# Kernel tuning notes

Measured on AMD Instinct MI355X. Metric: run time of the kernel, lower is better.

## Reference

```python
import jax, jax.numpy as jnp
import numpy as np

B, D = 4096, 128
LU, LI = 10, 20
NU, NI = 100000, 100000
NFU, NFI = 2000, 5000
MARGIN = 1.0


def setup_inputs() -> dict:
    key = jax.random.key(0)
    ks = jax.random.split(key, 32)
    s = 0.05
    n = lambda i, shape: (jax.random.normal(ks[i], shape, dtype=jnp.float32) * s)
    inp = {
        'user_indices': jax.random.randint(ks[0], (B,), 0, NU),
        'user_feat': jax.random.randint(ks[1], (B, LU), 0, NFU),
        'pos_item_indices': jax.random.randint(ks[2], (B,), 0, NI),
        'pos_item_feat': jax.random.randint(ks[3], (B, LI), 0, NFI),
        'neg_item_indices': jax.random.randint(ks[4], (B, 1), 0, NI),
        'neg_item_feat': jax.random.randint(ks[5], (B, 1, LI), 0, NFI),
        'comp_neg_indices': jax.random.randint(ks[6], (B,), 0, NI),
        'eps': jax.random.normal(ks[7], (B, D), dtype=jnp.float32),
        # learned parameters
        'emb_user': n(8, (NU, D)),
        'emb_item': n(9, (NI, D)),
        'emb_feat_user': n(10, (NFU, D)).at[0].set(0.0),  # row 0 is padding
        'emb_feat_item': n(11, (NFI, D)).at[0].set(0.0),
        'pop_emb_user': n(12, (D,)),
        'int_emb_user': n(13, (D,)),
        'pop_emb_item': n(14, (D,)),
        'int_emb_item': n(15, (D,)),
        'W_pop': n(16, (D, D)), 'b_pop': jnp.zeros((D,), jnp.float32),
        'W_int': n(17, (D, D)), 'b_int': jnp.zeros((D,), jnp.float32),
        'enc_W': n(18, (LI * D, D)), 'enc_b': jnp.zeros((D,), jnp.float32),
        'dec_W': n(19, (D, LI * D)), 'dec_b': jnp.zeros((LI * D,), jnp.float32),
        'fc11_W': n(20, (D, D)), 'fc11_b': jnp.zeros((D,), jnp.float32),
        'fc12_W': n(21, (D, D)), 'fc12_b': jnp.zeros((D,), jnp.float32),
    }
    return inp


def _attend_pool(fuse, feat_mask, vec, W, b):
    # fuse: [B, L+1, D], feat_mask: [B, L+1] (int, 0 = padded)
    scores = jnp.einsum('bld,d->bl', fuse, vec)
    scores = jnp.where(feat_mask == 0, -jnp.inf, scores)
    w = jax.nn.softmax(scores, axis=1)
    pooled = jnp.einsum('bld,bl->bd', fuse, w)
    return pooled @ W + b


def _branch(idx, feat, emb_table, feat_table, pop_vec, int_vec, W_pop, b_pop, W_int, b_int):
    e = emb_table[idx]                       # [B, D]
    fe = feat_table[feat]                    # [B, L, D]
    fuse = jnp.concatenate([e[:, None, :], fe], axis=1)           # [B, L+1, D]
    ones = jnp.ones((idx.shape[0], 1), dtype=feat.dtype)
    mask = jnp.concatenate([ones, feat], axis=1)                  # [B, L+1]
    hot = _attend_pool(fuse, mask, pop_vec, W_pop, b_pop)
    cold = _attend_pool(fuse, mask, int_vec, W_int, b_int)
    return hot, cold, e, fe


def reference(user_indices, user_feat, pos_item_indices, pos_item_feat,
              neg_item_indices, neg_item_feat, comp_neg_indices, eps,
              emb_user, emb_item, emb_feat_user, emb_feat_item,
              pop_emb_user, int_emb_user, pop_emb_item, int_emb_item,
              W_pop, b_pop, W_int, b_int,
              enc_W, enc_b, dec_W, dec_b, fc11_W, fc11_b, fc12_W, fc12_b):
    neg_item_indices = neg_item_indices.squeeze(1)
    neg_item_feat = neg_item_feat.squeeze(1)

    u_hot, u_cold, _, _ = _branch(user_indices, user_feat, emb_user, emb_feat_user,
                                  pop_emb_user, int_emb_user, W_pop, b_pop, W_int, b_int)
    p_hot, p_cold, pos_e, pos_fe = _branch(pos_item_indices, pos_item_feat, emb_item, emb_feat_item,
                                           pop_emb_item, int_emb_item, W_pop, b_pop, W_int, b_int)
    n_hot, n_cold, _, _ = _branch(neg_item_indices, neg_item_feat, emb_item, emb_feat_item,
                                  pop_emb_item, int_emb_item, W_pop, b_pop, W_int, b_int)

    loss_hot = jax.nn.relu(jnp.sum((u_hot - p_hot) ** 2, -1)
                           - jnp.sum((u_hot - n_hot) ** 2, -1) + MARGIN)
    loss_cold = jax.nn.relu(jnp.sum((u_cold - p_cold) ** 2, -1)
                            - jnp.sum((u_cold - n_cold) ** 2, -1) + MARGIN)

    # VAE over positive item feature embeddings
    x = pos_fe.reshape(pos_fe.shape[0], LI * D)
    h1 = jax.nn.relu(x @ enc_W + enc_b)
    mu = h1 @ fc11_W + fc11_b
    logvar = h1 @ fc12_W + fc12_b
    z = eps * jnp.exp(0.5 * logvar) + mu
    recon = z @ dec_W + dec_b                                    # [B, LI*D]
    mse = jnp.sum((recon - x) ** 2)
    kld = -0.5 * jnp.sum(1.0 + logvar - mu ** 2 - jnp.exp(logvar))
    vae_l = mse / LI + kld

    comp_e = emb_item[comp_neg_indices]
    mmi = -jnp.sum(jax.nn.log_sigmoid(jnp.sum(z * pos_e, 1) - jnp.sum(z * comp_e, 1)))
    item_vae_loss = mmi + vae_l + jnp.sum((z - pos_e) ** 2)

    return loss_hot, loss_cold, item_vae_loss
```

## Files before the change

### kernel.cpp

```cpp
#include <hip/hip_runtime.h>
#include <math.h>

#define BATCH 4096
#define DIM 128
#define LU 10
#define LI 20

typedef float  f32x4  __attribute__((ext_vector_type(4)));
typedef short  s16x8  __attribute__((ext_vector_type(8)));

__device__ __forceinline__ short f2bf(float x) {
    unsigned u = __float_as_uint(x);
    u += 0x7FFFu + ((u >> 16) & 1u);
    return (short)(u >> 16);
}
__device__ __forceinline__ float bf2f(unsigned short u) {
    return __uint_as_float(((unsigned)u) << 16);
}

__global__ __launch_bounds__(256) void k_prep(
    const float* __restrict__ enc_W, const float* __restrict__ dec_W,
    const float* __restrict__ fc11_W, const float* __restrict__ fc12_W,
    const float* __restrict__ W_pop, const float* __restrict__ W_int,
    const float* __restrict__ ef_item, const float* __restrict__ ef_user,
    short* __restrict__ encWT, short* __restrict__ decWT,
    short* __restrict__ fc11WT, short* __restrict__ fc12WT,
    short* __restrict__ wpopT, short* __restrict__ wintT,
    short* __restrict__ ef16, short* __restrict__ efU16)
{
    __shared__ float tile[32][33];
    const int b = blockIdx.x;
    const int t = threadIdx.x;

    if (b < 704) {
        const float* src; short* dst; int r0, c0, src_ld, dst_ld;
        if (b < 320) {
            int tk = b % 80, tj = b / 80;
            src = enc_W; dst = encWT; r0 = tk * 32; c0 = tj * 32; src_ld = 128; dst_ld = 2560;
        } else if (b < 640) {
            int tb = b - 320; int tc = tb % 80, td = tb / 80;
            src = dec_W; dst = decWT; r0 = td * 32; c0 = tc * 32; src_ld = 2560; dst_ld = 128;
        } else if (b < 656) {
            int tb = b - 640; int tk = tb % 4, tj = tb / 4;
            src = fc11_W; dst = fc11WT; r0 = tk * 32; c0 = tj * 32; src_ld = 128; dst_ld = 128;
        } else if (b < 672) {
            int tb = b - 656; int tk = tb % 4, tj = tb / 4;
            src = fc12_W; dst = fc12WT; r0 = tk * 32; c0 = tj * 32; src_ld = 128; dst_ld = 128;
        } else if (b < 688) {
            int tb = b - 672; int tk = tb % 4, tj = tb / 4;
            src = W_pop; dst = wpopT; r0 = tk * 32; c0 = tj * 32; src_ld = 128; dst_ld = 128;
        } else {
            int tb = b - 688; int tk = tb % 4, tj = tb / 4;
            src = W_int; dst = wintT; r0 = tk * 32; c0 = tj * 32; src_ld = 128; dst_ld = 128;
        }
        for (int q = 0; q < 4; ++q) {
            int e = t + q * 256;
            int r = e >> 5, c = e & 31;
            tile[r][c] = src[(size_t)(r0 + r) * src_ld + (c0 + c)];
        }
        __syncthreads();
        for (int q = 0; q < 4; ++q) {
            int e = t + q * 256;
            int r = e >> 5, c = e & 31;
            dst[(size_t)(c0 + r) * dst_ld + (r0 + c)] = f2bf(tile[c][r]);
        }
    } else if (b < 1329) {
        int base = (b - 704) * 1024 + t * 4;
        float4 v = *(const float4*)(ef_item + base);
        short4 o;
        o.x = f2bf(v.x); o.y = f2bf(v.y); o.z = f2bf(v.z); o.w = f2bf(v.w);
        *(short4*)(ef16 + base) = o;
    } else {
        int base = (b - 1329) * 1024 + t * 4;
        float4 v = *(const float4*)(ef_user + base);
        short4 o;
        o.x = f2bf(v.x); o.y = f2bf(v.y); o.z = f2bf(v.z); o.w = f2bf(v.w);
        *(short4*)(efU16 + base) = o;
    }
}

template<int L>
__device__ __forceinline__ void pool_online(
    const int* __restrict__ idxp, const int* __restrict__ featp,
    const float* __restrict__ etab, const unsigned short* __restrict__ ftab16,
    const float* __restrict__ vpop, const float* __restrict__ vint,
    float* __restrict__ poolH, float* __restrict__ poolC,
    int i, int j32)
{
    const int d = j32 * 4;
    const float4 vp = *(const float4*)(vpop + d);
    const float4 vi = *(const float4*)(vint + d);

    int fidx[L];
#pragma unroll
    for (int l = 0; l < L; ++l) fidx[l] = featp[(size_t)i * L + l];

    const int idx = idxp[i];
    const float4 e0 = *(const float4*)(etab + (size_t)idx * DIM + d);

    float sH = e0.x * vp.x + e0.y * vp.y + e0.z * vp.z + e0.w * vp.w;
    float sC = e0.x * vi.x + e0.y * vi.y + e0.z * vi.z + e0.w * vi.w;
    sH += __shfl_xor(sH, 1, 64);  sC += __shfl_xor(sC, 1, 64);
    sH += __shfl_xor(sH, 2, 64);  sC += __shfl_xor(sC, 2, 64);
    sH += __shfl_xor(sH, 4, 64);  sC += __shfl_xor(sC, 4, 64);
    sH += __shfl_xor(sH, 8, 64);  sC += __shfl_xor(sC, 8, 64);
    sH += __shfl_xor(sH, 16, 64); sC += __shfl_xor(sC, 16, 64);

    float mH = sH, mC = sC;
    float sumH = 1.f, sumC = 1.f;
    float aHx = e0.x, aHy = e0.y, aHz = e0.z, aHw = e0.w;
    float aCx = e0.x, aCy = e0.y, aCz = e0.z, aCw = e0.w;

#pragma unroll
    for (int l = 0; l < L; ++l) {
        const int f = fidx[l];
        const ushort4 u = *(const ushort4*)(ftab16 + (size_t)f * DIM + d);
        const float rx = bf2f(u.x), ry = bf2f(u.y), rz = bf2f(u.z), rw = bf2f(u.w);

        float pH = rx * vp.x + ry * vp.y + rz * vp.z + rw * vp.w;
        float pC = rx * vi.x + ry * vi.y + rz * vi.z + rw * vi.w;
        pH += __shfl_xor(pH, 1, 64);  pC += __shfl_xor(pC, 1, 64);
        pH += __shfl_xor(pH, 2, 64);  pC += __shfl_xor(pC, 2, 64);
        pH += __shfl_xor(pH, 4, 64);  pC += __shfl_xor(pC, 4, 64);
        pH += __shfl_xor(pH, 8, 64);  pC += __shfl_xor(pC, 8, 64);
        pH += __shfl_xor(pH, 16, 64); pC += __shfl_xor(pC, 16, 64);

        const bool v = (f != 0);
        const float mH2 = v ? fmaxf(mH, pH) : mH;
        const float mC2 = v ? fmaxf(mC, pC) : mC;
        const float sclH = __expf(mH - mH2);
        const float sclC = __expf(mC - mC2);
        const float wH = v ? __expf(pH - mH2) : 0.f;
        const float wC = v ? __expf(pC - mC2) : 0.f;
        sumH = sumH * sclH + wH;
        sumC = sumC * sclC + wC;
        aHx = aHx * sclH + wH * rx;  aHy = aHy * sclH + wH * ry;
        aHz = aHz * sclH + wH * rz;  aHw = aHw * sclH + wH * rw;
        aCx = aCx * sclC + wC * rx;  aCy = aCy * sclC + wC * ry;
        aCz = aCz * sclC + wC * rz;  aCw = aCw * sclC + wC * rw;
        mH = mH2; mC = mC2;
    }

    const float rH = 1.f / sumH, rC = 1.f / sumC;
    float4 oH; oH.x = aHx * rH; oH.y = aHy * rH; oH.z = aHz * rH; oH.w = aHw * rH;
    float4 oC; oC.x = aCx * rC; oC.y = aCy * rC; oC.z = aCz * rC; oC.w = aCw * rC;
    *(float4*)(poolH + (size_t)i * DIM + d) = oH;
    *(float4*)(poolC + (size_t)i * DIM + d) = oC;
}

__global__ __launch_bounds__(256) void k_AB(
    const int* __restrict__ user_idx, const int* __restrict__ user_feat,
    const int* __restrict__ pos_idx,  const int* __restrict__ pos_feat,
    const int* __restrict__ neg_idx,  const int* __restrict__ neg_feat,
    const int* __restrict__ comp_idx,
    const float* __restrict__ emb_user, const float* __restrict__ emb_item,
    const float* __restrict__ pop_u, const float* __restrict__ int_u,
    const float* __restrict__ pop_i, const float* __restrict__ int_i,
    const float* __restrict__ eps,
    const float* __restrict__ enc_b,
    const float* __restrict__ fc11_b, const float* __restrict__ fc12_b,
    const short* __restrict__ encWT,
    const short* __restrict__ fc11WT, const short* __restrict__ fc12WT,
    const short* __restrict__ ef16, const short* __restrict__ efU16,
    float* __restrict__ pooled,
    short* __restrict__ zbuf, float* __restrict__ vae_part)
{
    __shared__ int   featsL[320];
    __shared__ int   spi[16], sci[16];
    __shared__ __align__(16) short hlds[2048];
    __shared__ float sdots[4][16][3];
    __shared__ float red[256];

    const int t    = threadIdx.x;
    const int w    = t >> 6;
    const int lane = t & 63;
    const int g    = lane >> 4;
    const int q    = lane & 15;
    const size_t SEC = (size_t)BATCH * DIM;

    if (blockIdx.x < 1536) {
        const int pb  = blockIdx.x;
        const int br  = pb >> 9;
        const int i   = (pb & 511) * 8 + (t >> 5);
        const int j32 = t & 31;
        if (br == 0) {
            pool_online<LU>(user_idx, user_feat, emb_user,
                            (const unsigned short*)efU16, pop_u, int_u,
                            pooled + 0 * SEC, pooled + 1 * SEC, i, j32);
        } else if (br == 1) {
            pool_online<LI>(pos_idx, pos_feat, emb_item,
                            (const unsigned short*)ef16, pop_i, int_i,
                            pooled + 2 * SEC, pooled + 3 * SEC, i, j32);
        } else {
            pool_online<LI>(neg_idx, neg_feat, emb_item,
                            (const unsigned short*)ef16, pop_i, int_i,
                            pooled + 4 * SEC, pooled + 5 * SEC, i, j32);
        }
        return;
    }

    const int sg = blockIdx.x - 1536;
    const int i0 = sg * 16;

    if (t < 16)      spi[t] = pos_idx[i0 + t];
    else if (t < 32) sci[t - 16] = comp_idx[i0 + t - 16];
    if (t < 256) featsL[t] = pos_feat[i0 * LI + t];
    if (t < 64)  featsL[256 + t] = pos_feat[i0 * LI + 256 + t];
    __syncthreads();

    const int j0 = w * 32 + q;
    const int j1 = j0 + 16;
    const short* bbase0 = encWT + (size_t)j0 * 2560 + g * 8;
    const short* bbase1 = encWT + (size_t)j1 * 2560 + g * 8;

    f32x4 acc0 = {0.f, 0.f, 0.f, 0.f};
    f32x4 acc1 = {0.f, 0.f, 0.f, 0.f};
    for (int l = 0; l < LI; ++l) {
        const int f = featsL[q * LI + l];
        const short* arow = ef16 + (size_t)f * DIM + g * 8;
#pragma unroll
        for (int dt = 0; dt < 4; ++dt) {
            const int koff = l * 128 + dt * 32;
            s16x8 a  = *(const s16x8*)(arow + dt * 32);
            s16x8 b0 = *(const s16x8*)(bbase0 + koff);
            s16x8 b1 = *(const s16x8*)(bbase1 + koff);
            acc0 = __builtin_amdgcn_mfma_f32_16x16x32_bf16(a, b0, acc0, 0, 0, 0);
            acc1 = __builtin_amdgcn_mfma_f32_16x16x32_bf16(a, b1, acc1, 0, 0, 0);
        }
    }

    {
        float eb0 = enc_b[j0], eb1 = enc_b[j1];
#pragma unroll
        for (int r = 0; r < 4; ++r) {
            int s = g * 4 + r;
            float h0 = acc0[r] + eb0; h0 = h0 > 0.f ? h0 : 0.f;
            float h1 = acc1[r] + eb1; h1 = h1 > 0.f ? h1 : 0.f;
            int swz = (s & 7) << 3;
            hlds[(s * 128 + j0) ^ swz] = f2bf(h0);
            hlds[(s * 128 + j1) ^ swz] = f2bf(h1);
        }
    }
    __syncthreads();

    const short* fb0_11 = fc11WT + (size_t)j0 * DIM + g * 8;
    const short* fb1_11 = fc11WT + (size_t)j1 * DIM + g * 8;
    const short* fb0_12 = fc12WT + (size_t)j0 * DIM + g * 8;
    const short* fb1_12 = fc12WT + (size_t)j1 * DIM + g * 8;

    f32x4 mu0 = {0.f,0.f,0.f,0.f}, mu1 = {0.f,0.f,0.f,0.f};
    f32x4 lv0 = {0.f,0.f,0.f,0.f}, lv1 = {0.f,0.f,0.f,0.f};
#pragma unroll
    for (int kt = 0; kt < 4; ++kt) {
        int sidx = (q * 128 + kt * 32 + g * 8) ^ ((q & 7) << 3);
        s16x8 a = *(const s16x8*)&hlds[sidx];
        s16x8 w11a = *(const s16x8*)(fb0_11 + kt * 32);
        s16x8 w11b = *(const s16x8*)(fb1_11 + kt * 32);
        s16x8 w12a = *(const s16x8*)(fb0_12 + kt * 32);
        s16x8 w12b = *(const s16x8*)(fb1_12 + kt * 32);
        mu0 = __builtin_amdgcn_mfma_f32_16x16x32_bf16(a, w11a, mu0, 0, 0, 0);
        mu1 = __builtin_amdgcn_mfma_f32_16x16x32_bf16(a, w11b, mu1, 0, 0, 0);
        lv0 = __builtin_amdgcn_mfma_f32_16x16x32_bf16(a, w12a, lv0, 0, 0, 0);
        lv1 = __builtin_amdgcn_mfma_f32_16x16x32_bf16(a, w12b, lv1, 0, 0, 0);
    }

    float b11_0 = fc11_b[j0], b11_1 = fc11_b[j1];
    float b12_0 = fc12_b[j0], b12_1 = fc12_b[j1];

    float kacc = 0.f;
#pragma unroll
    for (int r = 0; r < 4; ++r) {
        const int s = g * 4 + r;
        const int i = i0 + s;
        float m0 = mu0[r] + b11_0, m1 = mu1[r] + b11_1;
        float v0 = lv0[r] + b12_0, v1 = lv1[r] + b12_1;
        float e0 = eps[(size_t)i * DIM + j0];
        float e1 = eps[(size_t)i * DIM + j1];
        float z0 = e0 * expf(0.5f * v0) + m0;
        float z1 = e1 * expf(0.5f * v1) + m1;
        zbuf[(size_t)i * DIM + j0] = f2bf(z0);
        zbuf[(size_t)i * DIM + j1] = f2bf(z1);
        kacc += (1.f + v0 - m0 * m0 - expf(v0)) + (1.f + v1 - m1 * m1 - expf(v1));

        const size_t pb2 = (size_t)spi[s] * DIM;
        const size_t cb2 = (size_t)sci[s] * DIM;
        float pe0 = emb_item[pb2 + j0], pe1 = emb_item[pb2 + j1];
        float ce0 = emb_item[cb2 + j0], ce1 = emb_item[cb2 + j1];
        float zp = z0 * pe0 + z1 * pe1;
        float zc = z0 * ce0 + z1 * ce1;
        float d0 = z0 - pe0, d1 = z1 - pe1;
        float zq = d0 * d0 + d1 * d1;
        for (int mm = 8; mm >= 1; mm >>= 1) {
            zp += __shfl_xor(zp, mm, 64);
            zc += __shfl_xor(zc, mm, 64);
            zq += __shfl_xor(zq, mm, 64);
        }
        if (q == 0) {
            sdots[w][s][0] = zp;
            sdots[w][s][1] = zc;
            sdots[w][s][2] = zq;
        }
    }

    red[t] = -0.5f * kacc;
    __syncthreads();
    if (t < 16) {
        float zp = 0.f, zc = 0.f, zq = 0.f;
        for (int ww = 0; ww < 4; ++ww) {
            zp += sdots[ww][t][0];
            zc += sdots[ww][t][1];
            zq += sdots[ww][t][2];
        }
        float x = zp - zc;
        float ls = (x >= 0.f) ? -log1pf(expf(-x)) : (x - log1pf(expf(x)));
        red[t] += -ls + zq;
    }
    __syncthreads();
    for (int off = 128; off > 0; off >>= 1) {
        if (t < off) red[t] += red[t + off];
        __syncthreads();
    }
    if (t == 0) vae_part[sg] = red[0];
}

__global__ __launch_bounds__(256) void k_C(
    const float* __restrict__ pooled,
    const short* __restrict__ wpopT, const short* __restrict__ wintT,
    const int* __restrict__ pos_feat,
    const float* __restrict__ ef_item, const float* __restrict__ dec_b,
    const short* __restrict__ decWT, const short* __restrict__ zbuf,
    float* __restrict__ out_hot, float* __restrict__ out_cold,
    float* __restrict__ dec_part)
{
    __shared__ int   featsL[320];
    __shared__ float red[256];
    __shared__ float sArr[4][16];

    const int t    = threadIdx.x;
    const int w    = t >> 6;
    const int lane = t & 63;
    const int g    = lane >> 4;
    const int q    = lane & 15;

    if (blockIdx.x >= 2048) {
        const int i0 = (blockIdx.x - 2048) * 16;
        const int h     = w >> 1;
        const int other = (w & 1) + 1;
        const float* pu = pooled + (size_t)(0 * 2 + h) * BATCH * DIM;
        const float* po = pooled + (size_t)(other * 2 + h) * BATCH * DIM;
        const short* wT = h ? wintT : wpopT;

        s16x8 afr[4];
#pragma unroll
        for (int kt = 0; kt < 4; ++kt) {
            const size_t off = (size_t)(i0 + q) * DIM + kt * 32 + g * 8;
            f32x4 ua = *(const f32x4*)(pu + off);
            f32x4 ub = *(const f32x4*)(pu + off + 4);
            f32x4 oa = *(const f32x4*)(po + off);
            f32x4 ob = *(const f32x4*)(po + off + 4);
            s16x8 v;
            v[0] = f2bf(ua[0] - oa[0]); v[1] = f2bf(ua[1] - oa[1]);
            v[2] = f2bf(ua[2] - oa[2]); v[3] = f2bf(ua[3] - oa[3]);
            v[4] = f2bf(ub[0] - ob[0]); v[5] = f2bf(ub[1] - ob[1]);
            v[6] = f2bf(ub[2] - ob[2]); v[7] = f2bf(ub[3] - ob[3]);
            afr[kt] = v;
        }

        float sq0 = 0.f, sq1 = 0.f, sq2 = 0.f, sq3 = 0.f;
        for (int fr = 0; fr < 8; ++fr) {
            const short* bb = wT + (size_t)(fr * 16 + q) * DIM + g * 8;
            f32x4 acc = {0.f, 0.f, 0.f, 0.f};
#pragma unroll
            for (int kt = 0; kt < 4; ++kt) {
                s16x8 bfr = *(const s16x8*)(bb + kt * 32);
                acc = __builtin_amdgcn_mfma_f32_16x16x32_bf16(afr[kt], bfr, acc, 0, 0, 0);
            }
            sq0 += acc[0] * acc[0]; sq1 += acc[1] * acc[1];
            sq2 += acc[2] * acc[2]; sq3 += acc[3] * acc[3];
        }
        for (int m = 8; m >= 1; m >>= 1) {
            sq0 += __shfl_xor(sq0, m, 64);
            sq1 += __shfl_xor(sq1, m, 64);
            sq2 += __shfl_xor(sq2, m, 64);
            sq3 += __shfl_xor(sq3, m, 64);
        }
        if (q == 0) {
            sArr[w][g * 4 + 0] = sq0;
            sArr[w][g * 4 + 1] = sq1;
            sArr[w][g * 4 + 2] = sq2;
            sArr[w][g * 4 + 3] = sq3;
        }
        __syncthreads();
        if (t < 16) {
            float v = sArr[0][t] - sArr[1][t] + 1.0f;
            out_hot[i0 + t] = v > 0.f ? v : 0.f;
        } else if (t < 32) {
            int s = t - 16;
            float v = sArr[2][s] - sArr[3][s] + 1.0f;
            out_cold[i0 + s] = v > 0.f ? v : 0.f;
        }
        return;
    }

    const int db     = blockIdx.x;
    const int cchunk = db >> 8;
    const int sb     = db & 255;
    const int i0     = sb * 16;

    if (t < 256) featsL[t] = pos_feat[i0 * LI + t];
    if (t < 64)  featsL[256 + t] = pos_feat[i0 * LI + 256 + t];
    __syncthreads();

    s16x8 za[4];
#pragma unroll
    for (int kt = 0; kt < 4; ++kt)
        za[kt] = *(const s16x8*)(zbuf + (size_t)(i0 + q) * DIM + kt * 32 + g * 8);

    const int cw = cchunk * 320 + w * 80;

    s16x8 bb[5][4];
    float xs[5][4];
    float bias[5];
#pragma unroll
    for (int fp = 0; fp < 5; ++fp) {
        const int c = cw + fp * 16 + q;
        const short* bp = decWT + (size_t)c * DIM + g * 8;
#pragma unroll
        for (int kt = 0; kt < 4; ++kt)
            bb[fp][kt] = *(const s16x8*)(bp + kt * 32);
        const int l = c >> 7, dcol = c & 127;
#pragma unroll
        for (int r = 0; r < 4; ++r)
            xs[fp][r] = ef_item[(size_t)featsL[(g * 4 + r) * LI + l] * DIM + dcol];
        bias[fp] = dec_b[c];
    }

    float macc = 0.f;
#pragma unroll
    for (int fp = 0; fp < 5; ++fp) {
        f32x4 acc = {0.f, 0.f, 0.f, 0.f};
#pragma unroll
        for (int kt = 0; kt < 4; ++kt)
            acc = __builtin_amdgcn_mfma_f32_16x16x32_bf16(za[kt], bb[fp][kt], acc, 0, 0, 0);
#pragma unroll
        for (int r = 0; r < 4; ++r) {
            float dd = acc[r] + bias[fp] - xs[fp][r];
            macc += dd * dd;
        }
    }

    red[t] = macc;
    __syncthreads();
    for (int off = 128; off > 0; off >>= 1) {
        if (t < off) red[t] += red[t + off];
        __syncthreads();
    }
    if (t == 0) dec_part[db] = red[0];
}

__global__ __launch_bounds__(256) void k_E(
    const float* __restrict__ vae_part, const float* __restrict__ dec_part,
    float* __restrict__ out_scalar)
{
    __shared__ float red[256];
    const int t = threadIdx.x;
    float b3 = 0.f;
    for (int qq = t; qq < 2048; qq += 256) b3 += dec_part[qq];
    red[t] = vae_part[t] + 0.05f * b3;
    __syncthreads();
    for (int off = 128; off > 0; off >>= 1) {
        if (t < off) red[t] += red[t + off];
        __syncthreads();
    }
    if (t == 0) out_scalar[0] = red[0];
}

extern "C" void kernel_launch(void* const* d_in, const int* in_sizes, int n_in,
                              void* d_out, int out_size, void* d_ws, size_t ws_size,
                              hipStream_t stream) {
    const int*   user_idx  = (const int*)d_in[0];
    const int*   user_feat = (const int*)d_in[1];
    const int*   pos_idx   = (const int*)d_in[2];
    const int*   pos_feat  = (const int*)d_in[3];
    const int*   neg_idx   = (const int*)d_in[4];
    const int*   neg_feat  = (const int*)d_in[5];
    const int*   comp_idx  = (const int*)d_in[6];
    const float* eps       = (const float*)d_in[7];
    const float* emb_user  = (const float*)d_in[8];
    const float* emb_item  = (const float*)d_in[9];
    const float* ef_user   = (const float*)d_in[10];
    const float* ef_item   = (const float*)d_in[11];
    const float* pop_u     = (const float*)d_in[12];
    const float* int_u     = (const float*)d_in[13];
    const float* pop_i     = (const float*)d_in[14];
    const float* int_i     = (const float*)d_in[15];
    const float* W_pop     = (const float*)d_in[16];
    const float* W_int     = (const float*)d_in[18];
    const float* enc_W     = (const float*)d_in[20];
    const float* enc_b     = (const float*)d_in[21];
    const float* dec_W     = (const float*)d_in[22];
    const float* dec_b     = (const float*)d_in[23];
    const float* fc11_W    = (const float*)d_in[24];
    const float* fc11_b    = (const float*)d_in[25];
    const float* fc12_W    = (const float*)d_in[26];
    const float* fc12_b    = (const float*)d_in[27];

    float* out = (float*)d_out;
    char*  ws  = (char*)d_ws;

    short* encWT    = (short*)(ws);
    short* decWT    = (short*)(ws + 655360);
    short* fc11WT   = (short*)(ws + 1310720);
    short* fc12WT   = (short*)(ws + 1343488);
    short* wpopT    = (short*)(ws + 1376256);
    short* wintT    = (short*)(ws + 1409024);
    short* ef16     = (short*)(ws + 1441792);
    short* efU16    = (short*)(ws + 2721792);
    short* zbuf     = (short*)(ws + 3233792);
    float* pooled   = (float*)(ws + 4282368);
    float* vae_part = (float*)(ws + 16865280);
    float* dec_part = (float*)(ws + 16866304);

    k_prep<<<dim3(1579), dim3(256), 0, stream>>>(
        enc_W, dec_W, fc11_W, fc12_W, W_pop, W_int, ef_item, ef_user,
        encWT, decWT, fc11WT, fc12WT, wpopT, wintT, ef16, efU16);

    k_AB<<<dim3(1792), dim3(256), 0, stream>>>(
        user_idx, user_feat, pos_idx, pos_feat, neg_idx, neg_feat, comp_idx,
        emb_user, emb_item,
        pop_u, int_u, pop_i, int_i,
        eps, enc_b, fc11_b, fc12_b,
        encWT, fc11WT, fc12WT, ef16, efU16,
        pooled, zbuf, vae_part);

    k_C<<<dim3(2304), dim3(256), 0, stream>>>(
        pooled, wpopT, wintT, pos_feat, ef_item, dec_b, decWT, zbuf,
        out, out + BATCH, dec_part);

    k_E<<<dim3(1), dim3(256), 0, stream>>>(vae_part, dec_part, out + 2 * BATCH);
}
```

Baseline: 91.05 us.

## Restructure attention pooling to stage rows in LDS and drop user-feature bf16 pre-pass

The attention pooling path now gathers each sample's embedding and feature rows straight from the fp32 tables into shared memory as bf16. It then computes scores, a plain two-pass softmax and the weighted sum from shared memory, replacing the per-lane online softmax with its shuffle reductions. The user feature table no longer gets a separate bf16 conversion in k_prep, which removes 250 blocks and a workspace buffer. Pooling blocks now come after the VAE blocks in the grid, and both share one shared-memory union, which raises per-block LDS use. The gather reads fp32 (twice the bytes of the old bf16 table reads), and the pooling stage adds several block-wide barriers.

```diff
diff --git a/kernel.cpp b/kernel.cpp
--- a/kernel.cpp
+++ b/kernel.cpp
@@ -8,6 +8,7 @@
 
 typedef float  f32x4  __attribute__((ext_vector_type(4)));
 typedef short  s16x8  __attribute__((ext_vector_type(8)));
+typedef unsigned short u16x8 __attribute__((ext_vector_type(8)));
 
 __device__ __forceinline__ short f2bf(float x) {
     unsigned u = __float_as_uint(x);
@@ -22,11 +23,11 @@
     const float* __restrict__ enc_W, const float* __restrict__ dec_W,
     const float* __restrict__ fc11_W, const float* __restrict__ fc12_W,
     const float* __restrict__ W_pop, const float* __restrict__ W_int,
-    const float* __restrict__ ef_item, const float* __restrict__ ef_user,
+    const float* __restrict__ ef_item,
     short* __restrict__ encWT, short* __restrict__ decWT,
     short* __restrict__ fc11WT, short* __restrict__ fc12WT,
     short* __restrict__ wpopT, short* __restrict__ wintT,
-    short* __restrict__ ef16, short* __restrict__ efU16)
+    short* __restrict__ ef16)
 {
     __shared__ float tile[32][33];
     const int b = blockIdx.x;
@@ -64,89 +65,31 @@
             int r = e >> 5, c = e & 31;
             dst[(size_t)(c0 + r) * dst_ld + (r0 + c)] = f2bf(tile[c][r]);
         }
-    } else if (b < 1329) {
+    } else {
         int base = (b - 704) * 1024 + t * 4;
         float4 v = *(const float4*)(ef_item + base);
         short4 o;
         o.x = f2bf(v.x); o.y = f2bf(v.y); o.z = f2bf(v.z); o.w = f2bf(v.w);
         *(short4*)(ef16 + base) = o;
-    } else {
-        int base = (b - 1329) * 1024 + t * 4;
-        float4 v = *(const float4*)(ef_user + base);
-        short4 o;
-        o.x = f2bf(v.x); o.y = f2bf(v.y); o.z = f2bf(v.z); o.w = f2bf(v.w);
-        *(short4*)(efU16 + base) = o;
-    }
-}
-
-template<int L>
-__device__ __forceinline__ void pool_online(
-    const int* __restrict__ idxp, const int* __restrict__ featp,
-    const float* __restrict__ etab, const unsigned short* __restrict__ ftab16,
-    const float* __restrict__ vpop, const float* __restrict__ vint,
-    float* __restrict__ poolH, float* __restrict__ poolC,
-    int i, int j32)
-{
-    const int d = j32 * 4;
-    const float4 vp = *(const float4*)(vpop + d);
-    const float4 vi = *(const float4*)(vint + d);
-
-    int fidx[L];
-#pragma unroll
-    for (int l = 0; l < L; ++l) fidx[l] = featp[(size_t)i * L + l];
-
-    const int idx = idxp[i];
-    const float4 e0 = *(const float4*)(etab + (size_t)idx * DIM + d);
-
-    float sH = e0.x * vp.x + e0.y * vp.y + e0.z * vp.z + e0.w * vp.w;
-    float sC = e0.x * vi.x + e0.y * vi.y + e0.z * vi.z + e0.w * vi.w;
-    sH += __shfl_xor(sH, 1, 64);  sC += __shfl_xor(sC, 1, 64);
-    sH += __shfl_xor(sH, 2, 64);  sC += __shfl_xor(sC, 2, 64);
-    sH += __shfl_xor(sH, 4, 64);  sC += __shfl_xor(sC, 4, 64);
-    sH += __shfl_xor(sH, 8, 64);  sC += __shfl_xor(sC, 8, 64);
-    sH += __shfl_xor(sH, 16, 64); sC += __shfl_xor(sC, 16, 64);
-
-    float mH = sH, mC = sC;
-    float sumH = 1.f, sumC = 1.f;
-    float aHx = e0.x, aHy = e0.y, aHz = e0.z, aHw = e0.w;
-    float aCx = e0.x, aCy = e0.y, aCz = e0.z, aCw = e0.w;
-
-#pragma unroll
-    for (int l = 0; l < L; ++l) {
-        const int f = fidx[l];
-        const ushort4 u = *(const ushort4*)(ftab16 + (size_t)f * DIM + d);
-        const float rx = bf2f(u.x), ry = bf2f(u.y), rz = bf2f(u.z), rw = bf2f(u.w);
-
-        float pH = rx * vp.x + ry * vp.y + rz * vp.z + rw * vp.w;
-        float pC = rx * vi.x + ry * vi.y + rz * vi.z + rw * vi.w;
-        pH += __shfl_xor(pH, 1, 64);  pC += __shfl_xor(pC, 1, 64);
-        pH += __shfl_xor(pH, 2, 64);  pC += __shfl_xor(pC, 2, 64);
-        pH += __shfl_xor(pH, 4, 64);  pC += __shfl_xor(pC, 4, 64);
-        pH += __shfl_xor(pH, 8, 64);  pC += __shfl_xor(pC, 8, 64);
-        pH += __shfl_xor(pH, 16, 64); pC += __shfl_xor(pC, 16, 64);
-
-        const bool v = (f != 0);
-        const float mH2 = v ? fmaxf(mH, pH) : mH;
-        const float mC2 = v ? fmaxf(mC, pC) : mC;
-        const float sclH = __expf(mH - mH2);
-        const float sclC = __expf(mC - mC2);
-        const float wH = v ? __expf(pH - mH2) : 0.f;
-        const float wC = v ? __expf(pC - mC2) : 0.f;
-        sumH = sumH * sclH + wH;
-        sumC = sumC * sclC + wC;
-        aHx = aHx * sclH + wH * rx;  aHy = aHy * sclH + wH * ry;
-        aHz = aHz * sclH + wH * rz;  aHw = aHw * sclH + wH * rw;
-        aCx = aCx * sclC + wC * rx;  aCy = aCy * sclC + wC * ry;
-        aCz = aCz * sclC + wC * rz;  aCw = aCw * sclC + wC * rw;
-        mH = mH2; mC = mC2;
-    }
-
-    const float rH = 1.f / sumH, rC = 1.f / sumC;
-    float4 oH; oH.x = aHx * rH; oH.y = aHy * rH; oH.z = aHz * rH; oH.w = aHw * rH;
-    float4 oC; oC.x = aCx * rC; oC.y = aCy * rC; oC.z = aCz * rC; oC.w = aCw * rC;
-    *(float4*)(poolH + (size_t)i * DIM + d) = oH;
-    *(float4*)(poolC + (size_t)i * DIM + d) = oC;
-}
+    }
+}
+
+#define FSTRIDE 132
+
+struct PoolS {
+    int   featsL[168];
+    short fuse[8 * 21 * FSTRIDE];
+    float sc[8][21][2];
+    float wl[8][2][21];
+};
+struct VaeS {
+    int   featsL[320];
+    int   spi[16];
+    int   sci[16];
+    short hlds[2048];
+    float sdots[4][16][3];
+    float red[256];
+};
 
 __global__ __launch_bounds__(256) void k_AB(
     const int* __restrict__ user_idx, const int* __restrict__ user_feat,
@@ -154,6 +97,7 @@
     const int* __restrict__ neg_idx,  const int* __restrict__ neg_feat,
     const int* __restrict__ comp_idx,
     const float* __restrict__ emb_user, const float* __restrict__ emb_item,
+    const float* __restrict__ ef_user,  const float* __restrict__ ef_item,
     const float* __restrict__ pop_u, const float* __restrict__ int_u,
     const float* __restrict__ pop_i, const float* __restrict__ int_i,
     const float* __restrict__ eps,
@@ -161,16 +105,11 @@
     const float* __restrict__ fc11_b, const float* __restrict__ fc12_b,
     const short* __restrict__ encWT,
     const short* __restrict__ fc11WT, const short* __restrict__ fc12WT,
-    const short* __restrict__ ef16, const short* __restrict__ efU16,
+    const short* __restrict__ ef16,
     float* __restrict__ pooled,
     short* __restrict__ zbuf, float* __restrict__ vae_part)
 {
-    __shared__ int   featsL[320];
-    __shared__ int   spi[16], sci[16];
-    __shared__ __align__(16) short hlds[2048];
-    __shared__ float sdots[4][16][3];
-    __shared__ float red[256];
-
+    __shared__ __align__(16) char smraw[sizeof(PoolS)];
     const int t    = threadIdx.x;
     const int w    = t >> 6;
     const int lane = t & 63;
@@ -178,34 +117,121 @@
     const int q    = lane & 15;
     const size_t SEC = (size_t)BATCH * DIM;
 
-    if (blockIdx.x < 1536) {
-        const int pb  = blockIdx.x;
-        const int br  = pb >> 9;
-        const int i   = (pb & 511) * 8 + (t >> 5);
-        const int j32 = t & 31;
-        if (br == 0) {
-            pool_online<LU>(user_idx, user_feat, emb_user,
-                            (const unsigned short*)efU16, pop_u, int_u,
-                            pooled + 0 * SEC, pooled + 1 * SEC, i, j32);
-        } else if (br == 1) {
-            pool_online<LI>(pos_idx, pos_feat, emb_item,
-                            (const unsigned short*)ef16, pop_i, int_i,
-                            pooled + 2 * SEC, pooled + 3 * SEC, i, j32);
-        } else {
-            pool_online<LI>(neg_idx, neg_feat, emb_item,
-                            (const unsigned short*)ef16, pop_i, int_i,
-                            pooled + 4 * SEC, pooled + 5 * SEC, i, j32);
+    if (blockIdx.x >= 256) {
+        PoolS& P = *reinterpret_cast<PoolS*>(smraw);
+        const int pb = blockIdx.x - 256;
+        const int br = pb / 512;
+        const int sb = pb % 512;
+        const int i0 = sb * 8;
+
+        const int Lf    = (br == 0) ? LU : LI;
+        const int Lrows = Lf + 1;
+        const int* idxp  = (br == 0) ? user_idx : (br == 1 ? pos_idx : neg_idx);
+        const int* featp = (br == 0) ? user_feat : (br == 1 ? pos_feat : neg_feat);
+        const float* etab = (br == 0) ? emb_user : emb_item;
+        const float* ftab = (br == 0) ? ef_user  : ef_item;
+        const float* vpop = (br == 0) ? pop_u : pop_i;
+        const float* vint = (br == 0) ? int_u : int_i;
+
+        if (t < 168) {
+            int u = t / 21, s = t % 21;
+            int val = 0;
+            if (s == 0)       val = idxp[i0 + u];
+            else if (s <= Lf) val = featp[(size_t)(i0 + u) * Lf + (s - 1)];
+            P.featsL[t] = val;
+        }
+        __syncthreads();
+
+        const int epr = Lrows * 32;
+        for (int u = 0; u < 8; ++u) {
+            for (int e = t; e < epr; e += 256) {
+                const int l  = e >> 5;
+                const int c4 = e & 31;
+                const int fv = P.featsL[u * 21 + l];
+                const float* srcp = (l == 0)
+                    ? etab + (size_t)fv * DIM + c4 * 4
+                    : ftab + (size_t)fv * DIM + c4 * 4;
+                float4 vv = *(const float4*)srcp;
+                short* dst = &P.fuse[(u * Lrows + l) * FSTRIDE + c4 * 4];
+                dst[0] = f2bf(vv.x); dst[1] = f2bf(vv.y);
+                dst[2] = f2bf(vv.z); dst[3] = f2bf(vv.w);
+            }
+        }
+        __syncthreads();
+
+        {
+            const int u = t >> 5;
+            for (int s2 = 0; s2 < 2; ++s2) {
+                const int d2 = (t & 31) + s2 * 32;
+                if (d2 < Lrows * 2) {
+                    const int l = d2 >> 1, v = d2 & 1;
+                    const float* vec = v ? vint : vpop;
+                    const short* row = &P.fuse[(u * Lrows + l) * FSTRIDE];
+                    float acc = 0.f;
+#pragma unroll
+                    for (int j = 0; j < 16; ++j) {
+                        u16x8 fv = *(const u16x8*)(row + j * 8);
+                        f32x4 va = *(const f32x4*)(vec + j * 8);
+                        f32x4 vb = *(const f32x4*)(vec + j * 8 + 4);
+                        acc += bf2f(fv[0]) * va[0] + bf2f(fv[1]) * va[1]
+                             + bf2f(fv[2]) * va[2] + bf2f(fv[3]) * va[3]
+                             + bf2f(fv[4]) * vb[0] + bf2f(fv[5]) * vb[1]
+                             + bf2f(fv[6]) * vb[2] + bf2f(fv[7]) * vb[3];
+                    }
+                    P.sc[u][l][v] = acc;
+                }
+            }
+        }
+        __syncthreads();
+
+        if (t < 16) {
+            const int u = t >> 1, v = t & 1;
+            float m = P.sc[u][0][v];
+            for (int l = 1; l < Lrows; ++l)
+                if (P.featsL[u * 21 + l] != 0) m = fmaxf(m, P.sc[u][l][v]);
+            float sum = 0.f;
+            for (int l = 0; l < Lrows; ++l) {
+                bool valid = (l == 0) || (P.featsL[u * 21 + l] != 0);
+                float e = valid ? __expf(P.sc[u][l][v] - m) : 0.f;
+                P.wl[u][v][l] = e;
+                sum += e;
+            }
+            float r = 1.f / sum;
+            for (int l = 0; l < Lrows; ++l) P.wl[u][v][l] *= r;
+        }
+        __syncthreads();
+
+        {
+            const int u = t >> 5, v = (t >> 4) & 1, c = t & 15;
+            const short* base = &P.fuse[u * Lrows * FSTRIDE + c * 8];
+            float o0 = 0.f, o1 = 0.f, o2 = 0.f, o3 = 0.f;
+            float o4 = 0.f, o5 = 0.f, o6 = 0.f, o7 = 0.f;
+            for (int l = 0; l < Lrows; ++l) {
+                const float wl = P.wl[u][v][l];
+                u16x8 fv = *(const u16x8*)(base + l * FSTRIDE);
+                o0 += wl * bf2f(fv[0]); o1 += wl * bf2f(fv[1]);
+                o2 += wl * bf2f(fv[2]); o3 += wl * bf2f(fv[3]);
+                o4 += wl * bf2f(fv[4]); o5 += wl * bf2f(fv[5]);
+                o6 += wl * bf2f(fv[6]); o7 += wl * bf2f(fv[7]);
+            }
+            float* dst = pooled + (size_t)(br * 2 + v) * SEC
+                       + (size_t)(i0 + u) * DIM + c * 8;
+            float4 w0; w0.x = o0; w0.y = o1; w0.z = o2; w0.w = o3;
+            float4 w1; w1.x = o4; w1.y = o5; w1.z = o6; w1.w = o7;
+            *(float4*)(dst)     = w0;
+            *(float4*)(dst + 4) = w1;
         }
         return;
     }
 
-    const int sg = blockIdx.x - 1536;
+    VaeS& V = *reinterpret_cast<VaeS*>(smraw);
+    const int sg = blockIdx.x;
     const int i0 = sg * 16;
 
-    if (t < 16)      spi[t] = pos_idx[i0 + t];
-    else if (t < 32) sci[t - 16] = comp_idx[i0 + t - 16];
-    if (t < 256) featsL[t] = pos_feat[i0 * LI + t];
-    if (t < 64)  featsL[256 + t] = pos_feat[i0 * LI + 256 + t];
+    if (t < 16)      V.spi[t] = pos_idx[i0 + t];
+    else if (t < 32) V.sci[t - 16] = comp_idx[i0 + t - 16];
+    if (t < 256) V.featsL[t] = pos_feat[i0 * LI + t];
+    if (t < 64)  V.featsL[256 + t] = pos_feat[i0 * LI + 256 + t];
     __syncthreads();
 
     const int j0 = w * 32 + q;
@@ -216,7 +242,7 @@
     f32x4 acc0 = {0.f, 0.f, 0.f, 0.f};
     f32x4 acc1 = {0.f, 0.f, 0.f, 0.f};
     for (int l = 0; l < LI; ++l) {
-        const int f = featsL[q * LI + l];
+        const int f = V.featsL[q * LI + l];
         const short* arow = ef16 + (size_t)f * DIM + g * 8;
 #pragma unroll
         for (int dt = 0; dt < 4; ++dt) {
@@ -237,8 +263,8 @@
             float h0 = acc0[r] + eb0; h0 = h0 > 0.f ? h0 : 0.f;
             float h1 = acc1[r] + eb1; h1 = h1 > 0.f ? h1 : 0.f;
             int swz = (s & 7) << 3;
-            hlds[(s * 128 + j0) ^ swz] = f2bf(h0);
-            hlds[(s * 128 + j1) ^ swz] = f2bf(h1);
+            V.hlds[(s * 128 + j0) ^ swz] = f2bf(h0);
+            V.hlds[(s * 128 + j1) ^ swz] = f2bf(h1);
         }
     }
     __syncthreads();
@@ -253,7 +279,7 @@
 #pragma unroll
     for (int kt = 0; kt < 4; ++kt) {
         int sidx = (q * 128 + kt * 32 + g * 8) ^ ((q & 7) << 3);
-        s16x8 a = *(const s16x8*)&hlds[sidx];
+        s16x8 a = *(const s16x8*)&V.hlds[sidx];
         s16x8 w11a = *(const s16x8*)(fb0_11 + kt * 32);
         s16x8 w11b = *(const s16x8*)(fb1_11 + kt * 32);
         s16x8 w12a = *(const s16x8*)(fb0_12 + kt * 32);
@@ -282,8 +308,8 @@
         zbuf[(size_t)i * DIM + j1] = f2bf(z1);
         kacc += (1.f + v0 - m0 * m0 - expf(v0)) + (1.f + v1 - m1 * m1 - expf(v1));
 
-        const size_t pb2 = (size_t)spi[s] * DIM;
-        const size_t cb2 = (size_t)sci[s] * DIM;
+        const size_t pb2 = (size_t)V.spi[s] * DIM;
+        const size_t cb2 = (size_t)V.sci[s] * DIM;
         float pe0 = emb_item[pb2 + j0], pe1 = emb_item[pb2 + j1];
         float ce0 = emb_item[cb2 + j0], ce1 = emb_item[cb2 + j1];
         float zp = z0 * pe0 + z1 * pe1;
@@ -296,31 +322,31 @@
             zq += __shfl_xor(zq, mm, 64);
         }
         if (q == 0) {
-            sdots[w][s][0] = zp;
-            sdots[w][s][1] = zc;
-            sdots[w][s][2] = zq;
-        }
-    }
-
-    red[t] = -0.5f * kacc;
+            V.sdots[w][s][0] = zp;
+            V.sdots[w][s][1] = zc;
+            V.sdots[w][s][2] = zq;
+        }
+    }
+
+    V.red[t] = -0.5f * kacc;
     __syncthreads();
     if (t < 16) {
         float zp = 0.f, zc = 0.f, zq = 0.f;
         for (int ww = 0; ww < 4; ++ww) {
-            zp += sdots[ww][t][0];
-            zc += sdots[ww][t][1];
-            zq += sdots[ww][t][2];
+            zp += V.sdots[ww][t][0];
+            zc += V.sdots[ww][t][1];
+            zq += V.sdots[ww][t][2];
         }
         float x = zp - zc;
         float ls = (x >= 0.f) ? -log1pf(expf(-x)) : (x - log1pf(expf(x)));
-        red[t] += -ls + zq;
+        V.red[t] += -ls + zq;
     }
     __syncthreads();
     for (int off = 128; off > 0; off >>= 1) {
-        if (t < off) red[t] += red[t + off];
-        __syncthreads();
-    }
-    if (t == 0) vae_part[sg] = red[0];
+        if (t < off) V.red[t] += V.red[t + off];
+        __syncthreads();
+    }
+    if (t == 0) vae_part[sg] = V.red[0];
 }
 
 __global__ __launch_bounds__(256) void k_C(
@@ -515,22 +541,21 @@
     short* wpopT    = (short*)(ws + 1376256);
     short* wintT    = (short*)(ws + 1409024);
     short* ef16     = (short*)(ws + 1441792);
-    short* efU16    = (short*)(ws + 2721792);
-    short* zbuf     = (short*)(ws + 3233792);
-    float* pooled   = (float*)(ws + 4282368);
-    float* vae_part = (float*)(ws + 16865280);
-    float* dec_part = (float*)(ws + 16866304);
-
-    k_prep<<<dim3(1579), dim3(256), 0, stream>>>(
-        enc_W, dec_W, fc11_W, fc12_W, W_pop, W_int, ef_item, ef_user,
-        encWT, decWT, fc11WT, fc12WT, wpopT, wintT, ef16, efU16);
+    short* zbuf     = (short*)(ws + 2721792);
+    float* pooled   = (float*)(ws + 3770368);
+    float* vae_part = (float*)(ws + 16353280);
+    float* dec_part = (float*)(ws + 16354304);
+
+    k_prep<<<dim3(1329), dim3(256), 0, stream>>>(
+        enc_W, dec_W, fc11_W, fc12_W, W_pop, W_int, ef_item,
+        encWT, decWT, fc11WT, fc12WT, wpopT, wintT, ef16);
 
     k_AB<<<dim3(1792), dim3(256), 0, stream>>>(
         user_idx, user_feat, pos_idx, pos_feat, neg_idx, neg_feat, comp_idx,
-        emb_user, emb_item,
+        emb_user, emb_item, ef_user, ef_item,
         pop_u, int_u, pop_i, int_i,
         eps, enc_b, fc11_b, fc12_b,
-        encWT, fc11WT, fc12WT, ef16, efU16,
+        encWT, fc11WT, fc12WT, ef16,
         pooled, zbuf, vae_part);
 
     k_C<<<dim3(2304), dim3(256), 0, stream>>>(
```

Result: slower. 119.4 us (+31.2%).
